# Optimization experiments

Measured on AMD Instinct MI355X. Metric: run time of the kernel, lower is better.

The kernel has to match this reference:

```python
import jax, jax.numpy as jnp
import numpy as np

E = 1024
FF = 4096
EPS = 1e-5


def _linear(x, W, b):
    # x: [B,S,in], W: [in,out], b: [out]
    return jnp.einsum('bsi,io->bso', x, W) + b


def _layernorm(x, g, b):
    mu = jnp.mean(x, axis=-1, keepdims=True)
    var = jnp.mean(jnp.square(x - mu), axis=-1, keepdims=True)
    return (x - mu) * jax.lax.rsqrt(var + EPS) * g + b


def setup_inputs() -> dict:
    key = jax.random.key(0)
    ks = jax.random.split(key, 8)
    s = 0.02
    inp = {
        'src': jax.random.normal(ks[0], (4, 2048, E), dtype=jnp.float32),
        'Wq': jax.random.normal(ks[1], (E, E), dtype=jnp.float32) * s,
        'bq': jnp.zeros((E,), jnp.float32),
        'Wk': jax.random.normal(ks[2], (E, E), dtype=jnp.float32) * s,
        'bk': jnp.zeros((E,), jnp.float32),
        'Wv': jax.random.normal(ks[3], (E, E), dtype=jnp.float32) * s,
        'bv': jnp.zeros((E,), jnp.float32),
        'Wo': jax.random.normal(ks[4], (E, E), dtype=jnp.float32) * s,
        'bo': jnp.zeros((E,), jnp.float32),
        'W1': jax.random.normal(ks[5], (E, FF), dtype=jnp.float32) * s,
        'b1': jnp.zeros((FF,), jnp.float32),
        'W2': jax.random.normal(ks[6], (FF, E), dtype=jnp.float32) * s,
        'b2': jnp.zeros((E,), jnp.float32),
        'g1': jnp.ones((E,), jnp.float32),
        'be1': jnp.zeros((E,), jnp.float32),
        'g2': jnp.ones((E,), jnp.float32),
        'be2': jnp.zeros((E,), jnp.float32),
    }
    return inp


def reference(src, Wq, bq, Wk, bk, Wv, bv, Wo, bo, W1, b1, W2, b2, g1, be1, g2, be2):
    Q = _linear(src, Wq, bq)
    K = _linear(src, Wk, bk)
    V = _linear(src, Wv, bv)
    # Single-head attention, NO 1/sqrt(d) scaling (faithful to source)
    scores = jnp.einsum('bqe,bke->bqk', Q, K)  # [B,S,S]
    weights = jax.nn.softmax(scores, axis=-1)
    attn = jnp.einsum('bqk,bke->bqe', weights, V)
    attn = _linear(attn, Wo, bo)
    x = _layernorm(src + attn, g1, be1)
    ff = _linear(x, W1, b1)
    ff = jax.nn.relu(ff)
    ff = _linear(ff, W2, b2)
    return _layernorm(x + ff, g2, be2)
```

## Files before the change

### kernel.cpp

```cpp
#include <hip/hip_runtime.h>
#include <hip/hip_bf16.h>


using u16 = unsigned short;
typedef __attribute__((ext_vector_type(8))) _Float16 half8;
typedef __attribute__((ext_vector_type(4))) float f32x4;

#define BATCH 4
#define SEQ   2048
#define EMB   1024
#define FFD   4096

#define SWZ(r) ((((r) >> 1) & 3) << 4)

__device__ __forceinline__ u16 f2h(float f) {
    union { _Float16 h; u16 u; } x;
    x.h = (_Float16)f;
    return x.u;
}
__device__ __forceinline__ float h2f(u16 u) {
    union { u16 u; _Float16 h; } x;
    x.u = u;
    return (float)x.h;
}

typedef const __attribute__((address_space(1))) void* gas_ptr;
typedef __attribute__((address_space(3))) void* las_ptr;

__device__ __forceinline__ void load_lds16(const void* g, void* l) {
    __builtin_amdgcn_global_load_lds((gas_ptr)g, (las_ptr)l, 16, 0, 0);
}

template <int BM, typename OutT, bool RELU, bool BIAS>
__global__ __launch_bounds__(512, 2) void gemm_q(
    const u16* __restrict__ A, const u16* __restrict__ Bt,
    OutT* __restrict__ C, const float* __restrict__ bias,
    int N, int K, int lda, int ldb, int ldc, long sA, long sB, long sC)
{
    constexpr int MF = BM / 32;
    constexpr int MH = MF / 2;
    constexpr int AL = BM / 128;
    constexpr int SLAB_A = BM * 32;
    constexpr int SLAB_B = 256 * 32;

    __shared__ u16 ldsA[4 * SLAB_A];
    __shared__ u16 ldsB[4 * SLAB_B];

    A  += (long)blockIdx.z * sA;
    Bt += (long)blockIdx.z * sB;
    C  += (long)blockIdx.z * sC;

    const int tid  = threadIdx.x;
    const int lane = tid & 63;
    const int wv   = tid >> 6;
    const int wm   = wv >> 2;
    const int wn   = wv & 3;
    const long row0 = (long)blockIdx.x * BM;
    const long col0 = (long)blockIdx.y * 256;

    long aoff[AL]; int adst[AL];
#pragma unroll
    for (int i = 0; i < AL; ++i) {
        const int d16 = i * 512 + tid;
        const int row = d16 >> 2;
        const int colb = ((d16 & 3) << 4) ^ SWZ(row);
        aoff[i] = (row0 + row) * (long)lda + (colb >> 1);
        adst[i] = d16 * 16;
    }
    long boff[2]; int bdst[2];
#pragma unroll
    for (int i = 0; i < 2; ++i) {
        const int d16 = i * 512 + tid;
        const int row = d16 >> 2;
        const int colb = ((d16 & 3) << 4) ^ SWZ(row);
        boff[i] = (col0 + row) * (long)ldb + (colb >> 1);
        bdst[i] = d16 * 16;
    }

    const int klane = (lane >> 4) << 4;
    const int arow = wm * (BM / 2) + (lane & 15);
    const int aro0 = arow * 64 + (klane ^ SWZ(arow));
    const int brow = wn * 64 + (lane & 15);
    const int bro0 = brow * 64 + (klane ^ SWZ(brow));

    f32x4 acc[MF][4] = {};
    half8 Aa[MH], Ab[MH], Ba[4], Bb[4];
    const int G = K >> 5;

    auto stage = [&](int g) {
        const int slot = g & 3;
        const long k0 = (long)g << 5;
#pragma unroll
        for (int i = 0; i < AL; ++i)
            load_lds16(A + aoff[i] + k0, (char*)ldsA + slot * (SLAB_A * 2) + adst[i]);
#pragma unroll
        for (int i = 0; i < 2; ++i)
            load_lds16(Bt + boff[i] + k0, (char*)ldsB + slot * (SLAB_B * 2) + bdst[i]);
    };

#define LDSA_P(slot) ((const char*)ldsA + (slot) * (SLAB_A * 2))
#define LDSB_P(slot) ((const char*)ldsB + (slot) * (SLAB_B * 2))
#define RD_A(dst, slot, mh)                                                   \
    _Pragma("unroll") for (int i_ = 0; i_ < MH; ++i_)                         \
        dst[i_] = *(const half8*)(LDSA_P(slot) + aro0 + ((mh) * MH + i_) * 1024);
#define RD_B(dst, slot)                                                       \
    _Pragma("unroll") for (int n_ = 0; n_ < 4; ++n_)                          \
        dst[n_] = *(const half8*)(LDSB_P(slot) + bro0 + n_ * 1024);
#define MM(Ax, Bx, mh)                                                        \
    __builtin_amdgcn_s_setprio(1);                                            \
    _Pragma("unroll") for (int i_ = 0; i_ < MH; ++i_)                         \
    _Pragma("unroll") for (int n_ = 0; n_ < 4; ++n_)                          \
        acc[(mh) * MH + i_][n_] = __builtin_amdgcn_mfma_f32_16x16x32_f16(     \
            Ax[i_], Bx[n_], acc[(mh) * MH + i_], 0, 0, 0)[0 * 0],             \
    (void)0;                                                                  \
    __builtin_amdgcn_s_setprio(0);
#undef MM
#define MM(Ax, Bx, mh)                                                        \
    __builtin_amdgcn_s_setprio(1);                                            \
    _Pragma("unroll") for (int i_ = 0; i_ < MH; ++i_)                         \
    _Pragma("unroll") for (int n_ = 0; n_ < 4; ++n_)                          \
        acc[(mh) * MH + i_][n_] = __builtin_amdgcn_mfma_f32_16x16x32_f16(     \
            Ax[i_], Bx[n_], acc[(mh) * MH + i_][n_], 0, 0, 0);                \
    __builtin_amdgcn_s_setprio(0);
#define BAR { __builtin_amdgcn_s_barrier(); __builtin_amdgcn_sched_barrier(0); }
#define VMS  asm volatile("s_waitcnt vmcnt(8)" ::: "memory")
#define VMT  asm volatile("s_waitcnt vmcnt(4)" ::: "memory")
#define VM0  asm volatile("s_waitcnt vmcnt(0)" ::: "memory")

    stage(0); stage(1); stage(2);
    VMS; BAR;
    RD_A(Aa, 0, 0); RD_B(Ba, 0);

#define PAIR(S, DOSTG0, VMA, DOSTG1, VMB)                                     \
    {                                                                         \
        if (DOSTG0) stage((S) + 3);                                           \
        RD_A(Ab, (S) & 3, 1); VMA; MM(Aa, Ba, 0); BAR;                        \
        RD_A(Aa, ((S) + 1) & 3, 0); RD_B(Bb, ((S) + 1) & 3);                  \
        MM(Ab, Ba, 1); BAR;                                                   \
        if (DOSTG1) stage((S) + 4);                                           \
        RD_A(Ab, ((S) + 1) & 3, 1); VMB; MM(Aa, Bb, 0); BAR;                  \
        RD_A(Aa, ((S) + 2) & 3, 0); RD_B(Ba, ((S) + 2) & 3);                  \
        MM(Ab, Bb, 1); BAR;                                                   \
    }

    for (int s = 0; s <= G - 6; s += 2) PAIR(s, true, VMS, true, VMS)
    PAIR(G - 4, true, VMS, false, VMT)
    RD_A(Ab, (G - 2) & 3, 1); VM0; MM(Aa, Ba, 0); BAR;
    RD_A(Aa, (G - 1) & 3, 0); RD_B(Bb, (G - 1) & 3); MM(Ab, Ba, 1); BAR;
    RD_A(Ab, (G - 1) & 3, 1); MM(Aa, Bb, 0); BAR;
    MM(Ab, Bb, 1);
#undef PAIR

#pragma unroll
    for (int n = 0; n < 4; ++n) {
        const long col = col0 + wn * 64 + n * 16 + (lane & 15);
        const float bv_ = BIAS ? bias[col] : 0.0f;
#pragma unroll
        for (int m = 0; m < MF; ++m) {
            const long row = row0 + wm * (BM / 2) + m * 16 + ((lane >> 4) << 2);
#pragma unroll
            for (int r = 0; r < 4; ++r) {
                float v = acc[m][n][r] + bv_;
                if (RELU) v = fmaxf(v, 0.0f);
                if constexpr (sizeof(OutT) == 2)
                    C[(row + r) * (long)ldc + col] = f2h(v);
                else
                    C[(row + r) * (long)ldc + col] = v;
            }
        }
    }
#undef LDSA_P
#undef LDSB_P
#undef RD_A
#undef RD_B
#undef MM
#undef BAR
#undef VMS
#undef VMT
#undef VM0
}

template <int BM, typename OutT, bool RELU, bool BIAS>
__global__ __launch_bounds__(512, 2) void gemm_s(
    const u16* __restrict__ A, const u16* __restrict__ Bt,
    OutT* __restrict__ C, const float* __restrict__ bias,
    int N, int K, int lda, int ldb, int ldc, long sA, long sB, long sC)
{
    constexpr int MF = BM / 32;
    constexpr int AL = BM / 128;
    constexpr int SLAB_A = BM * 32;
    constexpr int SLAB_B = 256 * 32;

    __shared__ u16 ldsA[4 * SLAB_A];
    __shared__ u16 ldsB[4 * SLAB_B];

    A  += (long)blockIdx.z * sA;
    Bt += (long)blockIdx.z * sB;
    C  += (long)blockIdx.z * sC;

    const int tid  = threadIdx.x;
    const int lane = tid & 63;
    const int wv   = tid >> 6;
    const int wm   = wv >> 2;
    const int wn   = wv & 3;
    const long row0 = (long)blockIdx.x * BM;
    const long col0 = (long)blockIdx.y * 256;

    long aoff[AL]; int adst[AL];
#pragma unroll
    for (int i = 0; i < AL; ++i) {
        const int d16 = i * 512 + tid;
        const int row = d16 >> 2;
        const int colb = ((d16 & 3) << 4) ^ SWZ(row);
        aoff[i] = (row0 + row) * (long)lda + (colb >> 1);
        adst[i] = d16 * 16;
    }
    long boff[2]; int bdst[2];
#pragma unroll
    for (int i = 0; i < 2; ++i) {
        const int d16 = i * 512 + tid;
        const int row = d16 >> 2;
        const int colb = ((d16 & 3) << 4) ^ SWZ(row);
        boff[i] = (col0 + row) * (long)ldb + (colb >> 1);
        bdst[i] = d16 * 16;
    }

    int aro[MF], bro[4];
    const int klane = (lane >> 4) << 4;
#pragma unroll
    for (int m = 0; m < MF; ++m) {
        const int row = wm * (BM / 2) + m * 16 + (lane & 15);
        aro[m] = row * 64 + (klane ^ SWZ(row));
    }
#pragma unroll
    for (int n = 0; n < 4; ++n) {
        const int row = wn * 64 + n * 16 + (lane & 15);
        bro[n] = row * 64 + (klane ^ SWZ(row));
    }

    f32x4 acc[MF][4] = {};
    const int G = K >> 5;

    auto stage = [&](int g) {
        const int slot = g & 3;
        const long k0 = (long)g << 5;
#pragma unroll
        for (int i = 0; i < AL; ++i)
            load_lds16(A + aoff[i] + k0, (char*)ldsA + slot * (SLAB_A * 2) + adst[i]);
#pragma unroll
        for (int i = 0; i < 2; ++i)
            load_lds16(Bt + boff[i] + k0, (char*)ldsB + slot * (SLAB_B * 2) + bdst[i]);
    };

#define VMS asm volatile("s_waitcnt vmcnt(6)" ::: "memory")
#define VMT asm volatile("s_waitcnt vmcnt(3)" ::: "memory")
#define VM0 asm volatile("s_waitcnt vmcnt(0)" ::: "memory")
#define VMNONE ((void)0)

#define GBODY(g, VMASM, DOSTAGE)                                              \
    {                                                                         \
        const int slot_ = (g) & 3;                                            \
        const char* abase_ = (const char*)ldsA + slot_ * (SLAB_A * 2);        \
        const char* bbase_ = (const char*)ldsB + slot_ * (SLAB_B * 2);        \
        half8 a_[MF], b_[4];                                                  \
        _Pragma("unroll") for (int m = 0; m < MF; ++m)                        \
            a_[m] = *(const half8*)(abase_ + aro[m]);                         \
        _Pragma("unroll") for (int n = 0; n < 4; ++n)                         \
            b_[n] = *(const half8*)(bbase_ + bro[n]);                         \
        if (DOSTAGE) stage((g) + 3);                                          \
        VMASM;                                                                \
        __builtin_amdgcn_s_setprio(1);                                        \
        _Pragma("unroll") for (int m = 0; m < MF; ++m)                        \
            _Pragma("unroll") for (int n = 0; n < 4; ++n)                     \
                acc[m][n] = __builtin_amdgcn_mfma_f32_16x16x32_f16(           \
                    a_[m], b_[n], acc[m][n], 0, 0, 0);                        \
        __builtin_amdgcn_s_setprio(0);                                        \
        __builtin_amdgcn_s_barrier();                                         \
        __builtin_amdgcn_sched_barrier(0);                                    \
    }

    stage(0); stage(1); stage(2);
    VMS;
    __builtin_amdgcn_s_barrier();
    __builtin_amdgcn_sched_barrier(0);

    for (int g = 0; g < G - 3; ++g) GBODY(g, VMS, true)
    GBODY(G - 3, VMT, false)
    GBODY(G - 2, VM0, false)
    GBODY(G - 1, VMNONE, false)
#undef GBODY
#undef VMS
#undef VMT
#undef VM0
#undef VMNONE

#pragma unroll
    for (int n = 0; n < 4; ++n) {
        const long col = col0 + wn * 64 + n * 16 + (lane & 15);
        const float bv_ = BIAS ? bias[col] : 0.0f;
#pragma unroll
        for (int m = 0; m < MF; ++m) {
            const long row = row0 + wm * (BM / 2) + m * 16 + ((lane >> 4) << 2);
#pragma unroll
            for (int r = 0; r < 4; ++r) {
                float v = acc[m][n][r] + bv_;
                if (RELU) v = fmaxf(v, 0.0f);
                if constexpr (sizeof(OutT) == 2)
                    C[(row + r) * (long)ldc + col] = f2h(v);
                else
                    C[(row + r) * (long)ldc + col] = v;
            }
        }
    }
}

__global__ __launch_bounds__(256) void transpose_cast(
    const float* __restrict__ in, u16* __restrict__ out, int R, int C)
{
    __shared__ float t[32][33];
    const int bc = blockIdx.x * 32, br = blockIdx.y * 32;
    const int lx = threadIdx.x & 31, ly = threadIdx.x >> 5;
#pragma unroll
    for (int i = 0; i < 32; i += 8)
        t[ly + i][lx] = in[(long)(br + ly + i) * C + bc + lx];
    __syncthreads();
#pragma unroll
    for (int i = 0; i < 32; i += 8)
        out[(long)(bc + ly + i) * R + br + lx] = f2h(t[lx][ly + i]);
}

__global__ __launch_bounds__(256) void transpose_h(
    const u16* __restrict__ in, u16* __restrict__ out,
    int ldin, int ldout, long sIn, long sOut)
{
    __shared__ u16 t[32][33];
    in  += (long)blockIdx.z * sIn;
    out += (long)blockIdx.z * sOut;
    const int bc = blockIdx.x * 32, br = blockIdx.y * 32;
    const int lx = threadIdx.x & 31, ly = threadIdx.x >> 5;
#pragma unroll
    for (int i = 0; i < 32; i += 8)
        t[ly + i][lx] = in[(long)(br + ly + i) * ldin + bc + lx];
    __syncthreads();
#pragma unroll
    for (int i = 0; i < 32; i += 8)
        out[(long)(bc + ly + i) * ldout + br + lx] = t[lx][ly + i];
}

__global__ __launch_bounds__(256) void cast_h(
    const float* __restrict__ in, u16* __restrict__ out)
{
    const long i = ((long)blockIdx.x * 256 + threadIdx.x) * 8;
    const float4 a = ((const float4*)(in + i))[0];
    const float4 b = ((const float4*)(in + i))[1];
    union { u16 u[8]; uint4 v; } pk;
    pk.u[0] = f2h(a.x); pk.u[1] = f2h(a.y); pk.u[2] = f2h(a.z); pk.u[3] = f2h(a.w);
    pk.u[4] = f2h(b.x); pk.u[5] = f2h(b.y); pk.u[6] = f2h(b.z); pk.u[7] = f2h(b.w);
    *(uint4*)(out + i) = pk.v;
}

__global__ __launch_bounds__(256) void concat_bias(
    const float* __restrict__ bq, const float* __restrict__ bk,
    const float* __restrict__ bv, float* __restrict__ o)
{
    const int i = blockIdx.x * 256 + threadIdx.x;
    o[i] = i < 1024 ? bq[i] : (i < 2048 ? bk[i - 1024] : bv[i - 2048]);
}

__global__ __launch_bounds__(256) void softmax_kernel(
    const u16* __restrict__ S, u16* __restrict__ P)
{
    const long row = blockIdx.x;
    const int tid = threadIdx.x;

    union { uint4 v; u16 u[8]; } in;
    in.v = ((const uint4*)(S + row * SEQ))[tid];
    float f[8];
#pragma unroll
    for (int j = 0; j < 8; ++j) f[j] = h2f(in.u[j]);

    float m = fmaxf(fmaxf(fmaxf(f[0], f[1]), fmaxf(f[2], f[3])),
                    fmaxf(fmaxf(f[4], f[5]), fmaxf(f[6], f[7])));
#pragma unroll
    for (int off = 32; off; off >>= 1) m = fmaxf(m, __shfl_xor(m, off));

    __shared__ float rm[4], rs[4];
    if ((tid & 63) == 0) rm[tid >> 6] = m;
    __syncthreads();
    m = fmaxf(fmaxf(rm[0], rm[1]), fmaxf(rm[2], rm[3]));

    float e[8], s = 0.0f;
#pragma unroll
    for (int j = 0; j < 8; ++j) { e[j] = expf(f[j] - m); s += e[j]; }
#pragma unroll
    for (int off = 32; off; off >>= 1) s += __shfl_xor(s, off);
    if ((tid & 63) == 0) rs[tid >> 6] = s;
    __syncthreads();
    s = (rs[0] + rs[1]) + (rs[2] + rs[3]);

    const float inv = 1.0f / s;
    union { u16 u[8]; uint4 v; } pk;
#pragma unroll
    for (int j = 0; j < 8; ++j) pk.u[j] = f2h(e[j] * inv);
    *(uint4*)(P + row * SEQ + tid * 8) = pk.v;
}

__global__ __launch_bounds__(256) void ln_kernel(
    const float* __restrict__ Ain, const float* __restrict__ Bin,
    const float* __restrict__ g, const float* __restrict__ be,
    float* __restrict__ Xout, u16* __restrict__ Xh)
{
    const long row = blockIdx.x;
    const int tid = threadIdx.x;

    const float4 a = ((const float4*)(Ain + row * EMB))[tid];
    const float4 b = ((const float4*)(Bin + row * EMB))[tid];
    const float h0 = a.x + b.x, h1 = a.y + b.y, h2 = a.z + b.z, h3 = a.w + b.w;

    float s = (h0 + h1) + (h2 + h3);
    float q = (h0 * h0 + h1 * h1) + (h2 * h2 + h3 * h3);
#pragma unroll
    for (int off = 32; off; off >>= 1) {
        s += __shfl_xor(s, off);
        q += __shfl_xor(q, off);
    }
    __shared__ float rsm[4], rqm[4];
    if ((tid & 63) == 0) { rsm[tid >> 6] = s; rqm[tid >> 6] = q; }
    __syncthreads();
    s = (rsm[0] + rsm[1]) + (rsm[2] + rsm[3]);
    q = (rqm[0] + rqm[1]) + (rqm[2] + rqm[3]);

    const float mu  = s * (1.0f / EMB);
    const float var = q * (1.0f / EMB) - mu * mu;
    const float rstd = rsqrtf(var + 1e-5f);

    const float4 gv = ((const float4*)g)[tid];
    const float4 bv = ((const float4*)be)[tid];
    const float y0 = (h0 - mu) * rstd * gv.x + bv.x;
    const float y1 = (h1 - mu) * rstd * gv.y + bv.y;
    const float y2 = (h2 - mu) * rstd * gv.z + bv.z;
    const float y3 = (h3 - mu) * rstd * gv.w + bv.w;

    ((float4*)(Xout + row * EMB))[tid] = make_float4(y0, y1, y2, y3);
    if (Xh) {
        union { u16 u[4]; uint2 v; } pk;
        pk.u[0] = f2h(y0); pk.u[1] = f2h(y1);
        pk.u[2] = f2h(y2); pk.u[3] = f2h(y3);
        ((uint2*)(Xh + row * EMB))[tid] = pk.v;
    }
}

extern "C" void kernel_launch(void* const* d_in, const int* in_sizes, int n_in,
                              void* d_out, int out_size, void* d_ws, size_t ws_size,
                              hipStream_t stream)
{
    const float* src = (const float*)d_in[0];
    const float* Wq  = (const float*)d_in[1];
    const float* bq  = (const float*)d_in[2];
    const float* Wk  = (const float*)d_in[3];
    const float* bk  = (const float*)d_in[4];
    const float* Wv  = (const float*)d_in[5];
    const float* bv  = (const float*)d_in[6];
    const float* Wo  = (const float*)d_in[7];
    const float* bo  = (const float*)d_in[8];
    const float* W1  = (const float*)d_in[9];
    const float* b1  = (const float*)d_in[10];
    const float* W2  = (const float*)d_in[11];
    const float* b2  = (const float*)d_in[12];
    const float* g1  = (const float*)d_in[13];
    const float* be1 = (const float*)d_in[14];
    const float* g2  = (const float*)d_in[15];
    const float* be2 = (const float*)d_in[16];
    float* out = (float*)d_out;

    char* ws = (char*)d_ws;
    const size_t MB = 1ull << 20;
    u16*   WqkvT   = (u16*)  (ws + 0 * MB);
    u16*   WoT     = (u16*)  (ws + 6 * MB);
    u16*   W1T     = (u16*)  (ws + 8 * MB);
    u16*   W2T     = (u16*)  (ws + 16 * MB);
    float* bqkv    = (float*)(ws + 24 * MB);
    u16*   Xh      = (u16*)  (ws + 25 * MB);
    u16*   QKVh    = (u16*)  (ws + 41 * MB);
    u16*   Vt      = (u16*)  (ws + 89 * MB);
    u16*   scoresh = (u16*)  (ws + 105 * MB);
    u16*   P       = (u16*)  (ws + 137 * MB);
    u16*   attn    = (u16*)  (ws + 105 * MB);
    float* attnp   = (float*)(ws + 121 * MB);
    float* x       = (float*)(ws + 153 * MB);
    u16*   xh      = (u16*)  (ws + 41 * MB);
    u16*   ff1     = (u16*)  (ws + 57 * MB);
    float* ff2     = (float*)(ws + 121 * MB);

    const int M = BATCH * SEQ;
    const long SS = (long)SEQ * SEQ;

    transpose_cast<<<dim3(32, 32, 1), 256, 0, stream>>>(Wq, WqkvT, EMB, EMB);
    transpose_cast<<<dim3(32, 32, 1), 256, 0, stream>>>(Wk, WqkvT + 1024 * 1024, EMB, EMB);
    transpose_cast<<<dim3(32, 32, 1), 256, 0, stream>>>(Wv, WqkvT + 2048 * 1024, EMB, EMB);
    transpose_cast<<<dim3(32, 32, 1), 256, 0, stream>>>(Wo, WoT, EMB, EMB);
    transpose_cast<<<dim3(128, 32, 1), 256, 0, stream>>>(W1, W1T, EMB, FFD);
    transpose_cast<<<dim3(32, 128, 1), 256, 0, stream>>>(W2, W2T, FFD, EMB);
    concat_bias<<<dim3(12), 256, 0, stream>>>(bq, bk, bv, bqkv);

    cast_h<<<dim3((M * EMB) / (256 * 8)), 256, 0, stream>>>(src, Xh);

    gemm_q<256, u16, false, true><<<dim3(32, 12, 1), 512, 0, stream>>>(
        Xh, WqkvT, QKVh, bqkv, 3072, 1024, 1024, 1024, 3072, 0, 0, 0);

    transpose_h<<<dim3(32, 64, BATCH), 256, 0, stream>>>(
        QKVh + 2048, Vt, 3072, SEQ, (long)SEQ * 3072, (long)EMB * SEQ);

    gemm_q<256, u16, false, false><<<dim3(8, 8, BATCH), 512, 0, stream>>>(
        QKVh, QKVh + 1024, scoresh, nullptr, SEQ, EMB, 3072, 3072, SEQ,
        (long)SEQ * 3072, (long)SEQ * 3072, SS);

    softmax_kernel<<<dim3(M), 256, 0, stream>>>(scoresh, P);

    gemm_s<128, u16, false, false><<<dim3(16, 4, BATCH), 512, 0, stream>>>(
        P, Vt, attn, nullptr, EMB, SEQ, SEQ, SEQ, EMB,
        SS, (long)EMB * SEQ, (long)SEQ * EMB);

    gemm_s<128, float, false, true><<<dim3(64, 4, 1), 512, 0, stream>>>(
        attn, WoT, attnp, bo, EMB, EMB, EMB, EMB, EMB, 0, 0, 0);

    ln_kernel<<<dim3(M), 256, 0, stream>>>(src, attnp, g1, be1, x, xh);

    gemm_q<256, u16, true, true><<<dim3(32, 16, 1), 512, 0, stream>>>(
        xh, W1T, ff1, b1, FFD, EMB, EMB, EMB, FFD, 0, 0, 0);

    gemm_s<128, float, false, true><<<dim3(64, 4, 1), 512, 0, stream>>>(
        ff1, W2T, ff2, b2, EMB, FFD, FFD, FFD, EMB, 0, 0, 0);

    ln_kernel<<<dim3(M), 256, 0, stream>>>(x, ff2, g2, be2, out, nullptr);
}
```

Baseline: 459.6 us.

## Replace 256x256 GEMM with 8-phase double-buffered K=64 pipeline

```diff
diff --git a/kernel.cpp b/kernel.cpp
--- a/kernel.cpp
+++ b/kernel.cpp
@@ -31,20 +31,14 @@
     __builtin_amdgcn_global_load_lds((gas_ptr)g, (las_ptr)l, 16, 0, 0);
 }
 
-template <int BM, typename OutT, bool RELU, bool BIAS>
-__global__ __launch_bounds__(512, 2) void gemm_q(
+template <typename OutT, bool RELU, bool BIAS>
+__global__ __launch_bounds__(512, 2) void gemm_8p(
     const u16* __restrict__ A, const u16* __restrict__ Bt,
     OutT* __restrict__ C, const float* __restrict__ bias,
     int N, int K, int lda, int ldb, int ldc, long sA, long sB, long sC)
 {
-    constexpr int MF = BM / 32;
-    constexpr int MH = MF / 2;
-    constexpr int AL = BM / 128;
-    constexpr int SLAB_A = BM * 32;
-    constexpr int SLAB_B = 256 * 32;
-
-    __shared__ u16 ldsA[4 * SLAB_A];
-    __shared__ u16 ldsB[4 * SLAB_B];
+    constexpr int BUF = 65536;
+    __shared__ __attribute__((aligned(16))) char lds[2 * BUF];
 
     A  += (long)blockIdx.z * sA;
     Bt += (long)blockIdx.z * sB;
@@ -55,133 +49,139 @@
     const int wv   = tid >> 6;
     const int wm   = wv >> 2;
     const int wn   = wv & 3;
-    const long row0 = (long)blockIdx.x * BM;
+    const long row0 = (long)blockIdx.x * 256;
     const long col0 = (long)blockIdx.y * 256;
 
-    long aoff[AL]; int adst[AL];
-#pragma unroll
-    for (int i = 0; i < AL; ++i) {
-        const int d16 = i * 512 + tid;
-        const int row = d16 >> 2;
-        const int colb = ((d16 & 3) << 4) ^ SWZ(row);
-        aoff[i] = (row0 + row) * (long)lda + (colb >> 1);
-        adst[i] = d16 * 16;
-    }
-    long boff[2]; int bdst[2];
+    long aS[2], bS[2]; int dD[2];
 #pragma unroll
     for (int i = 0; i < 2; ++i) {
         const int d16 = i * 512 + tid;
-        const int row = d16 >> 2;
-        const int colb = ((d16 & 3) << 4) ^ SWZ(row);
-        boff[i] = (col0 + row) * (long)ldb + (colb >> 1);
-        bdst[i] = d16 * 16;
-    }
-
-    const int klane = (lane >> 4) << 4;
-    const int arow = wm * (BM / 2) + (lane & 15);
-    const int aro0 = arow * 64 + (klane ^ SWZ(arow));
-    const int brow = wn * 64 + (lane & 15);
-    const int bro0 = brow * 64 + (klane ^ SWZ(brow));
-
-    f32x4 acc[MF][4] = {};
-    half8 Aa[MH], Ab[MH], Ba[4], Bb[4];
-    const int G = K >> 5;
-
-    auto stage = [&](int g) {
-        const int slot = g & 3;
-        const long k0 = (long)g << 5;
-#pragma unroll
-        for (int i = 0; i < AL; ++i)
-            load_lds16(A + aoff[i] + k0, (char*)ldsA + slot * (SLAB_A * 2) + adst[i]);
-#pragma unroll
-        for (int i = 0; i < 2; ++i)
-            load_lds16(Bt + boff[i] + k0, (char*)ldsB + slot * (SLAB_B * 2) + bdst[i]);
-    };
-
-#define LDSA_P(slot) ((const char*)ldsA + (slot) * (SLAB_A * 2))
-#define LDSB_P(slot) ((const char*)ldsB + (slot) * (SLAB_B * 2))
-#define RD_A(dst, slot, mh)                                                   \
-    _Pragma("unroll") for (int i_ = 0; i_ < MH; ++i_)                         \
-        dst[i_] = *(const half8*)(LDSA_P(slot) + aro0 + ((mh) * MH + i_) * 1024);
-#define RD_B(dst, slot)                                                       \
-    _Pragma("unroll") for (int n_ = 0; n_ < 4; ++n_)                          \
-        dst[n_] = *(const half8*)(LDSB_P(slot) + bro0 + n_ * 1024);
-#define MM(Ax, Bx, mh)                                                        \
-    __builtin_amdgcn_s_setprio(1);                                            \
-    _Pragma("unroll") for (int i_ = 0; i_ < MH; ++i_)                         \
-    _Pragma("unroll") for (int n_ = 0; n_ < 4; ++n_)                          \
-        acc[(mh) * MH + i_][n_] = __builtin_amdgcn_mfma_f32_16x16x32_f16(     \
-            Ax[i_], Bx[n_], acc[(mh) * MH + i_], 0, 0, 0)[0 * 0],             \
-    (void)0;                                                                  \
-    __builtin_amdgcn_s_setprio(0);
-#undef MM
-#define MM(Ax, Bx, mh)                                                        \
-    __builtin_amdgcn_s_setprio(1);                                            \
-    _Pragma("unroll") for (int i_ = 0; i_ < MH; ++i_)                         \
-    _Pragma("unroll") for (int n_ = 0; n_ < 4; ++n_)                          \
-        acc[(mh) * MH + i_][n_] = __builtin_amdgcn_mfma_f32_16x16x32_f16(     \
-            Ax[i_], Bx[n_], acc[(mh) * MH + i_][n_], 0, 0, 0);                \
-    __builtin_amdgcn_s_setprio(0);
-#define BAR { __builtin_amdgcn_s_barrier(); __builtin_amdgcn_sched_barrier(0); }
-#define VMS  asm volatile("s_waitcnt vmcnt(8)" ::: "memory")
-#define VMT  asm volatile("s_waitcnt vmcnt(4)" ::: "memory")
-#define VM0  asm volatile("s_waitcnt vmcnt(0)" ::: "memory")
-
-    stage(0); stage(1); stage(2);
-    VMS; BAR;
-    RD_A(Aa, 0, 0); RD_B(Ba, 0);
-
-#define PAIR(S, DOSTG0, VMA, DOSTG1, VMB)                                     \
+        const int lrow = d16 >> 3;
+        const int sl   = d16 & 7;
+        const long cswz = (long)((sl ^ (lrow & 7)) << 3);
+        aS[i] = (row0 + lrow) * (long)lda + cswz;
+        bS[i] = (col0 + lrow) * (long)ldb + cswz;
+        dD[i] = d16 * 16;
+    }
+    const long aHop = 128 * (long)lda;
+    const long bHop = 128 * (long)ldb;
+
+    const int klb = (lane >> 4) << 4;
+    const int swz = (lane & 7) << 4;
+    const int aRB = (wm * 128 + (lane & 15)) * 128 + (klb ^ swz);
+    const int bRB = 32768 + (wn * 64 + (lane & 15)) * 128 + (klb ^ swz);
+
+    f32x4 acc[8][4] = {};
+    half8 a[8], b[4];
+    const int G = K >> 6;
+
+#define SGA(BUFB, H, KT)                                                      \
+    { _Pragma("unroll") for (int i_ = 0; i_ < 2; ++i_)                        \
+          load_lds16(A + aS[i_] + (H) * aHop + (long)(KT) * 64,               \
+                     lds + (BUFB) + (H) * 16384 + dD[i_]); }
+#define SGB(BUFB, H, KT)                                                      \
+    { _Pragma("unroll") for (int i_ = 0; i_ < 2; ++i_)                        \
+          load_lds16(Bt + bS[i_] + (H) * bHop + (long)(KT) * 64,              \
+                     lds + (BUFB) + 32768 + (H) * 16384 + dD[i_]); }
+#define NOP8 ((void)0)
+#define VM8 asm volatile("s_waitcnt vmcnt(8)" ::: "memory")
+#define VM6 asm volatile("s_waitcnt vmcnt(6)" ::: "memory")
+#define VM2 asm volatile("s_waitcnt vmcnt(2)" ::: "memory")
+#define VMZ asm volatile("s_waitcnt vmcnt(0)" ::: "memory")
+
+#define PH8(BUFB, QM, QN, RDA, RDB, STG, VM)                                  \
     {                                                                         \
-        if (DOSTG0) stage((S) + 3);                                           \
-        RD_A(Ab, (S) & 3, 1); VMA; MM(Aa, Ba, 0); BAR;                        \
-        RD_A(Aa, ((S) + 1) & 3, 0); RD_B(Bb, ((S) + 1) & 3);                  \
-        MM(Ab, Ba, 1); BAR;                                                   \
-        if (DOSTG1) stage((S) + 4);                                           \
-        RD_A(Ab, ((S) + 1) & 3, 1); VMB; MM(Aa, Bb, 0); BAR;                  \
-        RD_A(Aa, ((S) + 2) & 3, 0); RD_B(Ba, ((S) + 2) & 3);                  \
-        MM(Ab, Bb, 1); BAR;                                                   \
-    }
-
-    for (int s = 0; s <= G - 6; s += 2) PAIR(s, true, VMS, true, VMS)
-    PAIR(G - 4, true, VMS, false, VMT)
-    RD_A(Ab, (G - 2) & 3, 1); VM0; MM(Aa, Ba, 0); BAR;
-    RD_A(Aa, (G - 1) & 3, 0); RD_B(Bb, (G - 1) & 3); MM(Ab, Ba, 1); BAR;
-    RD_A(Ab, (G - 1) & 3, 1); MM(Aa, Bb, 0); BAR;
-    MM(Ab, Bb, 1);
-#undef PAIR
-
+        if (RDA) {                                                            \
+            _Pragma("unroll") for (int m_ = 0; m_ < 4; ++m_)                  \
+            _Pragma("unroll") for (int k_ = 0; k_ < 2; ++k_)                  \
+                a[m_ * 2 + k_] = *(const half8*)(lds + (BUFB) +               \
+                    ((aRB + (QM) * 8192 + m_ * 2048) ^ (k_ << 6)));           \
+        }                                                                     \
+        if (RDB) {                                                            \
+            _Pragma("unroll") for (int n_ = 0; n_ < 2; ++n_)                  \
+            _Pragma("unroll") for (int k_ = 0; k_ < 2; ++k_)                  \
+                b[n_ * 2 + k_] = *(const half8*)(lds + (BUFB) +               \
+                    ((bRB + (QN) * 4096 + n_ * 2048) ^ (k_ << 6)));           \
+        }                                                                     \
+        STG; VM;                                                              \
+        __builtin_amdgcn_s_barrier();                                         \
+        asm volatile("s_waitcnt lgkmcnt(0)" ::: "memory");                    \
+        __builtin_amdgcn_sched_barrier(0);                                    \
+        __builtin_amdgcn_s_setprio(1);                                        \
+        _Pragma("unroll") for (int k_ = 0; k_ < 2; ++k_)                      \
+        _Pragma("unroll") for (int m_ = 0; m_ < 4; ++m_)                      \
+        _Pragma("unroll") for (int n_ = 0; n_ < 2; ++n_)                      \
+            acc[(QM) * 4 + m_][(QN) * 2 + n_] =                               \
+                __builtin_amdgcn_mfma_f32_16x16x32_f16(                       \
+                    a[m_ * 2 + k_], b[n_ * 2 + k_],                           \
+                    acc[(QM) * 4 + m_][(QN) * 2 + n_], 0, 0, 0);              \
+        __builtin_amdgcn_s_setprio(0);                                        \
+        __builtin_amdgcn_s_barrier();                                         \
+    }
+
+    SGA(0, 0, 0); SGB(0, 1, 0); SGB(0, 0, 0); SGA(0, 1, 0);
+    SGA(BUF, 0, 1); SGB(BUF, 1, 1);
+    VM6;
+    __builtin_amdgcn_s_barrier();
+
+    for (int t = 0; t < G - 2; ++t) {
+        const int cb = (t & 1) * BUF, ob = cb ^ BUF;
+        PH8(cb, 0, 0, 1, 1, SGB(ob, 0, t + 1), NOP8)
+        PH8(cb, 0, 1, 0, 1, SGA(ob, 1, t + 1), VM8)
+        PH8(cb, 1, 1, 1, 0, SGA(cb, 0, t + 2), NOP8)
+        PH8(cb, 1, 0, 0, 1, SGB(cb, 1, t + 2), VM6)
+    }
+    {
+        const int cb = ((G - 2) & 1) * BUF, ob = cb ^ BUF;
+        PH8(cb, 0, 0, 1, 1, SGB(ob, 0, G - 1), NOP8)
+        PH8(cb, 0, 1, 0, 1, SGA(ob, 1, G - 1), VM8)
+        PH8(cb, 1, 1, 1, 0, NOP8, NOP8)
+        PH8(cb, 1, 0, 0, 1, NOP8, VM2)
+    }
+    {
+        const int cb = ((G - 1) & 1) * BUF;
+        PH8(cb, 0, 0, 1, 1, NOP8, NOP8)
+        PH8(cb, 0, 1, 0, 1, NOP8, VMZ)
+        PH8(cb, 1, 1, 1, 0, NOP8, NOP8)
+        PH8(cb, 1, 0, 0, 1, NOP8, NOP8)
+    }
+#undef PH8
+#undef SGA
+#undef SGB
+#undef NOP8
+#undef VM8
+#undef VM6
+#undef VM2
+#undef VMZ
+
+    long cofs[4]; float bb[4];
 #pragma unroll
     for (int n = 0; n < 4; ++n) {
-        const long col = col0 + wn * 64 + n * 16 + (lane & 15);
-        const float bv_ = BIAS ? bias[col] : 0.0f;
-#pragma unroll
-        for (int m = 0; m < MF; ++m) {
-            const long row = row0 + wm * (BM / 2) + m * 16 + ((lane >> 4) << 2);
-#pragma unroll
-            for (int r = 0; r < 4; ++r) {
-                float v = acc[m][n][r] + bv_;
+        cofs[n] = col0 + wn * 64 + (n >> 1) * 32 + (n & 1) * 16 + (lane & 15);
+        bb[n] = BIAS ? bias[cofs[n]] : 0.0f;
+    }
+#pragma unroll
+    for (int m = 0; m < 8; ++m) {
+#pragma unroll
+        for (int r = 0; r < 4; ++r) {
+            const long row = row0 + wm * 128 + (m >> 2) * 64 + (m & 3) * 16 +
+                             ((lane >> 4) << 2) + r;
+            OutT* Crow = C + row * (long)ldc;
+#pragma unroll
+            for (int n = 0; n < 4; ++n) {
+                float v = acc[m][n][r] + bb[n];
                 if (RELU) v = fmaxf(v, 0.0f);
                 if constexpr (sizeof(OutT) == 2)
-                    C[(row + r) * (long)ldc + col] = f2h(v);
+                    Crow[cofs[n]] = f2h(v);
                 else
-                    C[(row + r) * (long)ldc + col] = v;
+                    Crow[cofs[n]] = v;
             }
         }
     }
-#undef LDSA_P
-#undef LDSB_P
-#undef RD_A
-#undef RD_B
-#undef MM
-#undef BAR
-#undef VMS
-#undef VMT
-#undef VM0
 }
 
 template <int BM, typename OutT, bool RELU, bool BIAS>
-__global__ __launch_bounds__(512, 2) void gemm_s(
+__global__ __launch_bounds__(512, 2) void gemm_dp(
     const u16* __restrict__ A, const u16* __restrict__ Bt,
     OutT* __restrict__ C, const float* __restrict__ bias,
     int N, int K, int lda, int ldb, int ldc, long sA, long sB, long sC)
@@ -505,31 +505,31 @@
 
     cast_h<<<dim3((M * EMB) / (256 * 8)), 256, 0, stream>>>(src, Xh);
 
-    gemm_q<256, u16, false, true><<<dim3(32, 12, 1), 512, 0, stream>>>(
+    gemm_8p<u16, false, true><<<dim3(32, 12, 1), 512, 0, stream>>>(
         Xh, WqkvT, QKVh, bqkv, 3072, 1024, 1024, 1024, 3072, 0, 0, 0);
 
     transpose_h<<<dim3(32, 64, BATCH), 256, 0, stream>>>(
         QKVh + 2048, Vt, 3072, SEQ, (long)SEQ * 3072, (long)EMB * SEQ);
 
-    gemm_q<256, u16, false, false><<<dim3(8, 8, BATCH), 512, 0, stream>>>(
+    gemm_8p<u16, false, false><<<dim3(8, 8, BATCH), 512, 0, stream>>>(
         QKVh, QKVh + 1024, scoresh, nullptr, SEQ, EMB, 3072, 3072, SEQ,
         (long)SEQ * 3072, (long)SEQ * 3072, SS);
 
     softmax_kernel<<<dim3(M), 256, 0, stream>>>(scoresh, P);
 
-    gemm_s<128, u16, false, false><<<dim3(16, 4, BATCH), 512, 0, stream>>>(
+    gemm_dp<128, u16, false, false><<<dim3(16, 4, BATCH), 512, 0, stream>>>(
         P, Vt, attn, nullptr, EMB, SEQ, SEQ, SEQ, EMB,
         SS, (long)EMB * SEQ, (long)SEQ * EMB);
 
-    gemm_s<128, float, false, true><<<dim3(64, 4, 1), 512, 0, stream>>>(
+    gemm_dp<128, float, false, true><<<dim3(64, 4, 1), 512, 0, stream>>>(
         attn, WoT, attnp, bo, EMB, EMB, EMB, EMB, EMB, 0, 0, 0);
 
     ln_kernel<<<dim3(M), 256, 0, stream>>>(src, attnp, g1, be1, x, xh);
 
-    gemm_q<256, u16, true, true><<<dim3(32, 16, 1), 512, 0, stream>>>(
+    gemm_8p<u16, true, true><<<dim3(32, 16, 1), 512, 0, stream>>>(
         xh, W1T, ff1, b1, FFD, EMB, EMB, EMB, FFD, 0, 0, 0);
 
-    gemm_s<128, float, false, true><<<dim3(64, 4, 1), 512, 0, stream>>>(
+    gemm_dp<128, float, false, true><<<dim3(64, 4, 1), 512, 0, stream>>>(
         ff1, W2T, ff2, b2, EMB, FFD, FFD, FFD, EMB, 0, 0, 0);
 
     ln_kernel<<<dim3(M), 256, 0, stream>>>(x, ff2, g2, be2, out, nullptr);
```

After: 413.2 us. 10.1% less time.
